# Kernel tuning notes

Hardware: AMD Instinct MI355X
Metric: run time of the kernel (lower is better)

The kernel has to match this reference:

```python
import jax, jax.numpy as jnp
import numpy as np

K_STEPS = 2  # number of staged propagation levels encoded in edge_mask


def _propagate(h, src, dst, mask, num_nodes):
    """KPropagate: K staged scatter-add steps over the edge list.

    Step k sums messages along edges with edge_mask == k; later steps
    propagate the freshly aggregated values (rule-node fan-out).
    """
    out = jnp.zeros_like(h)
    cur = h
    for k in range(K_STEPS):
        msg = jnp.where((mask == k)[:, None], cur[src], jnp.zeros((), h.dtype))  # [E, F]
        out = out + jax.ops.segment_sum(msg, dst, num_segments=num_nodes)
        cur = out
    return out


def setup_inputs() -> dict:
    key = jax.random.key(0)
    ks = jax.random.split(key, 8)
    V, R = 50000, 10000
    N = V + R
    E = 160000
    F_IN, F_OUT = 512, 128
    x = jax.random.normal(ks[0], (N, F_IN), dtype=jnp.float32)
    edge_index = jax.random.randint(ks[1], (2, E), 0, N, dtype=jnp.int64)
    edge_mask = jax.random.randint(ks[2], (E,), 0, K_STEPS, dtype=jnp.int64)
    # lin1: in_features -> in_features; lin2: in_features -> out_features
    s1 = 1.0 / np.sqrt(F_IN)
    W1 = jax.random.uniform(ks[3], (F_IN, F_IN), jnp.float32, -s1, s1)
    b1 = jax.random.uniform(ks[4], (F_IN,), jnp.float32, -s1, s1)
    W2 = jax.random.uniform(ks[5], (F_IN, F_OUT), jnp.float32, -s1, s1)
    b2 = jax.random.uniform(ks[6], (F_OUT,), jnp.float32, -s1, s1)
    return {"x": x, "edge_index": edge_index, "edge_mask": edge_mask,
            "vertex_cnt": V, "rule_cnt": R,
            "W1": W1, "b1": b1, "W2": W2, "b2": b2}


def reference(x, edge_index, edge_mask, vertex_cnt, rule_cnt, W1, b1, W2, b2):
    N = x.shape[0]  # == vertex_cnt + rule_cnt
    src, dst = edge_index[0], edge_index[1]
    h = x @ W1 + b1                                   # lin1
    h = jax.nn.relu(_propagate(h, src, dst, edge_mask, N))  # P1 -> relu
    h = h @ W2 + b2                                   # lin2
    h = _propagate(h, src, dst, edge_mask, N)         # P2
    # NOTE: original code computes log_softmax into `out` but returns x (=h).
    return h
```

## Files before the change

### kernel.cpp

```cpp
#include <hip/hip_runtime.h>

typedef __bf16 bf16x8 __attribute__((ext_vector_type(8)));
typedef float  floatx4 __attribute__((ext_vector_type(4)));
typedef unsigned short ushortx8 __attribute__((ext_vector_type(8)));
typedef unsigned short ushortx4 __attribute__((ext_vector_type(4)));
typedef unsigned short ushortx2 __attribute__((ext_vector_type(2)));

__device__ __forceinline__ float bf2f(unsigned short u) {
    return __uint_as_float(((unsigned)u) << 16);
}
__device__ __forceinline__ unsigned short f2bf(float f) {
    unsigned u = __float_as_uint(f);
    return (unsigned short)((u + 0x7FFFu + ((u >> 16) & 1u)) >> 16);
}

__device__ __forceinline__ void gload_lds16(const unsigned short* g, unsigned short* l) {
    __builtin_amdgcn_global_load_lds(
        (const __attribute__((address_space(1))) void*)g,
        (__attribute__((address_space(3))) void*)l, 16, 0, 0);
}

__global__ void cvt_f32_bf16_kernel(const float* __restrict__ in,
                                    unsigned short* __restrict__ out, int n4) {
    int i = blockIdx.x * blockDim.x + threadIdx.x;
    if (i >= n4) return;
    float4 v = ((const float4*)in)[i];
    ushortx4 o;
    o[0] = f2bf(v.x); o[1] = f2bf(v.y); o[2] = f2bf(v.z); o[3] = f2bf(v.w);
    ((ushortx4*)out)[i] = o;
}

__global__ void transpose_cvt_kernel(const float* __restrict__ in,
                                     unsigned short* __restrict__ out,
                                     int K, int N) {
    int idx = blockIdx.x * blockDim.x + threadIdx.x;
    if (idx >= K * N) return;
    int k = idx / N, n = idx - k * N;
    out[n * K + k] = f2bf(in[idx]);
}

__global__ void init_head_kernel(int* __restrict__ head, int n) {
    int i = blockIdx.x * blockDim.x + threadIdx.x;
    if (i < n) head[i] = -1;
}

__global__ void build_list_kernel(const int* __restrict__ ei, const int* __restrict__ em,
                                  int E, int Nn,
                                  int* __restrict__ head, int* __restrict__ nxt) {
    int e = blockIdx.x * blockDim.x + threadIdx.x;
    if (e >= E) return;
    int d = ei[E + e];
    int m = em[e];
    nxt[e] = atomicExch(&head[m * Nn + d], e);
}

#define BM 128
#define BN 128
#define BK 64

__global__ __launch_bounds__(256) void gemm_bt_bias(
    const unsigned short* __restrict__ A,
    const unsigned short* __restrict__ Bt,
    const float* __restrict__ bias,
    unsigned short* __restrict__ C,
    int M, int N, int K)
{
    __shared__ unsigned short Sh[16384];
    unsigned short (*As)[512] = (unsigned short(*)[512])Sh;
    unsigned short (*Bs)[512] = (unsigned short(*)[512])(Sh + 8192);

    const int tid  = threadIdx.x;
    const int lane = tid & 63;
    const int wave = tid >> 6;

    int bx, by;
    if (gridDim.x == 4) {
        int id = blockIdx.y * 4 + blockIdx.x;
        int full = (gridDim.y & ~7) * 4;
        if (id < full) {
            bx = (id >> 3) & 3;
            by = (id >> 5) * 8 + (id & 7);
        } else {
            int t = id - full;
            by = (gridDim.y & ~7) + (t >> 2);
            bx = t & 3;
        }
    } else {
        bx = blockIdx.x; by = blockIdx.y;
    }
    const int bM = by * BM;
    const int bN = bx * BN;
    const int wm = (wave >> 1) * 64;
    const int wn = (wave & 1) * 64;
    const int q    = lane >> 4;
    const int mrow = lane & 15;

    const unsigned short* pA[4];
    const unsigned short* pB[4];
#pragma unroll
    for (int c = 0; c < 4; c++) {
        int gg = wave + 4 * c;
        int g7 = gg & 7, s = gg >> 3;
        int rA = bM + g7 * 16 + mrow; if (rA >= M) rA = M - 1;
        int rB = bN + g7 * 16 + mrow;
        pA[c] = A  + (size_t)rA * K + s * 32 + q * 8;
        pB[c] = Bt + (size_t)rB * K + s * 32 + q * 8;
    }

    floatx4 acc[4][4];
#pragma unroll
    for (int i = 0; i < 4; i++)
#pragma unroll
        for (int j = 0; j < 4; j++) acc[i][j] = (floatx4)(0.0f);

    for (int kt = 0; kt < K; kt += BK) {
#pragma unroll
        for (int c = 0; c < 4; c++) {
            gload_lds16(pA[c] + kt, &As[wave + 4 * c][0]);
            gload_lds16(pB[c] + kt, &Bs[wave + 4 * c][0]);
        }
        __syncthreads();

#pragma unroll
        for (int s = 0; s < 2; s++) {
            bf16x8 af[4], bfv[4];
#pragma unroll
            for (int mi = 0; mi < 4; mi++)
                af[mi] = *(const bf16x8*)&As[s * 8 + (wave >> 1) * 4 + mi][lane * 8];
#pragma unroll
            for (int ni = 0; ni < 4; ni++)
                bfv[ni] = *(const bf16x8*)&Bs[s * 8 + (wave & 1) * 4 + ni][lane * 8];
#pragma unroll
            for (int mi = 0; mi < 4; mi++)
#pragma unroll
                for (int ni = 0; ni < 4; ni++)
                    acc[mi][ni] = __builtin_amdgcn_mfma_f32_16x16x32_bf16(
                        af[mi], bfv[ni], acc[mi][ni], 0, 0, 0);
        }
        __syncthreads();
    }

    unsigned short* lbuf = Sh + wave * 2048;
    float bv[4];
#pragma unroll
    for (int ni = 0; ni < 4; ni++) bv[ni] = bias[bN + wn + ni * 16 + mrow];

#pragma unroll
    for (int p = 0; p < 2; p++) {
#pragma unroll
        for (int mh = 0; mh < 2; mh++) {
            int mi = 2 * p + mh;
#pragma unroll
            for (int ni = 0; ni < 4; ni++)
#pragma unroll
                for (int r = 0; r < 4; r++)
                    lbuf[(mh * 16 + q * 4 + r) * 64 + ni * 16 + mrow] =
                        f2bf(acc[mi][ni][r] + bv[ni]);
        }
#pragma unroll
        for (int i = 0; i < 4; i++) {
            int prow = i * 8 + (lane >> 3);
            int pcol = (lane & 7) * 8;
            int grow = bM + wm + p * 32 + prow;
            if (grow < M)
                *(ushortx8*)(C + (size_t)grow * N + bN + wn + pcol) =
                    *(const ushortx8*)&lbuf[prow * 64 + pcol];
        }
    }
}

template <int VEC> struct VecT;
template <> struct VecT<8> { typedef ushortx8 type; };
template <> struct VecT<2> { typedef ushortx2 type; };

template <int VEC, bool ADD_SELF, bool RELU, bool OUT_F32>
__global__ __launch_bounds__(256) void prop_step_kernel(
    const unsigned short* __restrict__ cur,
    void* __restrict__ outp,
    const int* __restrict__ head,
    const int* __restrict__ nxt,
    const int* __restrict__ esrc,
    int Nn)
{
    typedef typename VecT<VEC>::type VT;
    const int w = blockIdx.x * 4 + (threadIdx.x >> 6);
    if (w >= Nn) return;
    const int lane = threadIdx.x & 63;
    const int F = VEC * 64;
    const size_t off = (size_t)w * F + lane * VEC;

    float acc[VEC];
    if (ADD_SELF) {
        VT v = *(const VT*)(cur + off);
#pragma unroll
        for (int i = 0; i < VEC; i++) acc[i] = bf2f(v[i]);
    } else {
#pragma unroll
        for (int i = 0; i < VEC; i++) acc[i] = 0.0f;
    }

    for (int e = head[w]; e >= 0; e = nxt[e]) {
        int s = esrc[e];
        VT v = *(const VT*)(cur + (size_t)s * F + lane * VEC);
#pragma unroll
        for (int i = 0; i < VEC; i++) acc[i] += bf2f(v[i]);
    }

#pragma unroll
    for (int i = 0; i < VEC; i++)
        if (RELU && acc[i] < 0.0f) acc[i] = 0.0f;

    if (OUT_F32) {
        float* out = (float*)outp;
        float2 o2;
#pragma unroll
        for (int i = 0; i < VEC; i += 2) {
            o2.x = acc[i]; o2.y = acc[i + 1];
            *(float2*)(out + off + i) = o2;
        }
    } else {
        VT o;
#pragma unroll
        for (int i = 0; i < VEC; i++) o[i] = f2bf(acc[i]);
        *(VT*)((unsigned short*)outp + off) = o;
    }
}

extern "C" void kernel_launch(void* const* d_in, const int* in_sizes, int n_in,
                              void* d_out, int out_size, void* d_ws, size_t ws_size,
                              hipStream_t stream)
{
    const float* x  = (const float*)d_in[0];
    const int*   ei = (const int*)d_in[1];
    const int*   em = (const int*)d_in[2];
    const float* W1 = (const float*)d_in[5];
    const float* b1 = (const float*)d_in[6];
    const float* W2 = (const float*)d_in[7];
    const float* b2 = (const float*)d_in[8];

    const int FIN = 512, FOUT = 128;
    const int Nn = in_sizes[0] / FIN;
    const int E  = in_sizes[2];

    char* ws = (char*)d_ws;
    size_t off = 0;
    auto alloc = [&](size_t bytes) -> char* {
        char* p = ws + off;
        off += (bytes + 255) & ~(size_t)255;
        return p;
    };
    unsigned short* W1t = (unsigned short*)alloc((size_t)FIN * FIN * 2);
    unsigned short* W2t = (unsigned short*)alloc((size_t)FIN * FOUT * 2);
    unsigned short* xb  = (unsigned short*)alloc((size_t)Nn * FIN * 2);
    unsigned short* h1  = (unsigned short*)alloc((size_t)Nn * FIN * 2);
    unsigned short* h2  = (unsigned short*)alloc((size_t)Nn * FOUT * 2);
    unsigned short* A2  = (unsigned short*)alloc((size_t)Nn * FOUT * 2);
    int* head = (int*)alloc((size_t)2 * Nn * 4);
    int* nxt  = (int*)alloc((size_t)E * 4);
    unsigned short* A1 = xb;
    (void)ws_size; (void)n_in; (void)out_size;

    cvt_f32_bf16_kernel<<<((Nn * FIN / 4) + 255) / 256, 256, 0, stream>>>(x, xb, Nn * FIN / 4);
    transpose_cvt_kernel<<<(FIN * FIN + 255) / 256, 256, 0, stream>>>(W1, W1t, FIN, FIN);
    transpose_cvt_kernel<<<(FIN * FOUT + 255) / 256, 256, 0, stream>>>(W2, W2t, FIN, FOUT);

    init_head_kernel<<<(2 * Nn + 255) / 256, 256, 0, stream>>>(head, 2 * Nn);
    build_list_kernel<<<(E + 255) / 256, 256, 0, stream>>>(ei, em, E, Nn, head, nxt);

    {
        dim3 grid(FIN / BN, (Nn + BM - 1) / BM);
        gemm_bt_bias<<<grid, 256, 0, stream>>>(xb, W1t, b1, h1, Nn, FIN, FIN);
    }

    {
        int grid = (Nn + 3) / 4;
        prop_step_kernel<8, false, false, false><<<grid, 256, 0, stream>>>(h1, A1, head,      nxt, ei, Nn);
        prop_step_kernel<8, true,  true,  false><<<grid, 256, 0, stream>>>(A1, h1, head + Nn, nxt, ei, Nn);
    }

    {
        dim3 grid(FOUT / BN, (Nn + BM - 1) / BM);
        gemm_bt_bias<<<grid, 256, 0, stream>>>(h1, W2t, b2, h2, Nn, FOUT, FIN);
    }

    {
        int grid = (Nn + 3) / 4;
        prop_step_kernel<2, false, false, false><<<grid, 256, 0, stream>>>(h2, A2, head,      nxt, ei, Nn);
        prop_step_kernel<2, true,  false, true ><<<grid, 256, 0, stream>>>(A2, d_out, head + Nn, nxt, ei, Nn);
    }
}
```

Before: 398.3 us.

## Double-buffer LDS tiles in bf16 GEMM to overlap loads with MFMA

Splits the GEMM shared-memory tile into two A/B buffer pairs. The loop now issues async global-to-LDS loads for the next K tile while MFMAs run on the current one, with one wait-and-barrier per step instead of two. The goal is to hide global load latency behind compute. In exchange LDS use per block doubles, which can reduce occupancy, and the unrolled schedule assumes an even number of K tiles.

```diff
diff --git a/kernel.cpp b/kernel.cpp
--- a/kernel.cpp
+++ b/kernel.cpp
@@ -65,9 +65,10 @@
     unsigned short* __restrict__ C,
     int M, int N, int K)
 {
-    __shared__ unsigned short Sh[16384];
-    unsigned short (*As)[512] = (unsigned short(*)[512])Sh;
-    unsigned short (*Bs)[512] = (unsigned short(*)[512])(Sh + 8192);
+    __shared__ unsigned short BufA0[8192];
+    __shared__ unsigned short BufB0[8192];
+    __shared__ unsigned short BufA1[8192];
+    __shared__ unsigned short BufB1[8192];
 
     const int tid  = threadIdx.x;
     const int lane = tid & 63;
@@ -113,34 +114,61 @@
 #pragma unroll
         for (int j = 0; j < 4; j++) acc[i][j] = (floatx4)(0.0f);
 
-    for (int kt = 0; kt < K; kt += BK) {
-#pragma unroll
-        for (int c = 0; c < 4; c++) {
-            gload_lds16(pA[c] + kt, &As[wave + 4 * c][0]);
-            gload_lds16(pB[c] + kt, &Bs[wave + 4 * c][0]);
-        }
-        __syncthreads();
-
-#pragma unroll
-        for (int s = 0; s < 2; s++) {
-            bf16x8 af[4], bfv[4];
-#pragma unroll
-            for (int mi = 0; mi < 4; mi++)
-                af[mi] = *(const bf16x8*)&As[s * 8 + (wave >> 1) * 4 + mi][lane * 8];
-#pragma unroll
-            for (int ni = 0; ni < 4; ni++)
-                bfv[ni] = *(const bf16x8*)&Bs[s * 8 + (wave & 1) * 4 + ni][lane * 8];
-#pragma unroll
-            for (int mi = 0; mi < 4; mi++)
-#pragma unroll
-                for (int ni = 0; ni < 4; ni++)
-                    acc[mi][ni] = __builtin_amdgcn_mfma_f32_16x16x32_bf16(
-                        af[mi], bfv[ni], acc[mi][ni], 0, 0, 0);
-        }
-        __syncthreads();
-    }
-
-    unsigned short* lbuf = Sh + wave * 2048;
+#define STAGE(DA, DB, T) do {                                        \
+    const int ko_ = (T) * BK;                                        \
+    _Pragma("unroll")                                                \
+    for (int c_ = 0; c_ < 4; c_++) {                                 \
+        gload_lds16(pA[c_] + ko_, &DA[(wave + 4 * c_) * 512]);       \
+        gload_lds16(pB[c_] + ko_, &DB[(wave + 4 * c_) * 512]);       \
+    }                                                                \
+} while (0)
+
+#define COMPUTE(SA, SB) do {                                                   \
+    _Pragma("unroll")                                                          \
+    for (int s_ = 0; s_ < 2; s_++) {                                           \
+        bf16x8 af[4], bfv[4];                                                  \
+        _Pragma("unroll")                                                      \
+        for (int mi = 0; mi < 4; mi++)                                         \
+            af[mi] = *(const bf16x8*)&SA[(s_ * 8 + (wave >> 1) * 4 + mi) * 512 \
+                                         + lane * 8];                          \
+        _Pragma("unroll")                                                      \
+        for (int ni = 0; ni < 4; ni++)                                         \
+            bfv[ni] = *(const bf16x8*)&SB[(s_ * 8 + (wave & 1) * 4 + ni) * 512 \
+                                          + lane * 8];                         \
+        _Pragma("unroll")                                                      \
+        for (int mi = 0; mi < 4; mi++)                                         \
+            _Pragma("unroll")                                                  \
+            for (int ni = 0; ni < 4; ni++)                                     \
+                acc[mi][ni] = __builtin_amdgcn_mfma_f32_16x16x32_bf16(         \
+                    af[mi], bfv[ni], acc[mi][ni], 0, 0, 0);                    \
+    }                                                                          \
+} while (0)
+
+#define WB asm volatile("s_waitcnt vmcnt(0) lgkmcnt(0)\n\ts_barrier" ::: "memory")
+
+    const int NT = K / BK;
+
+    STAGE(BufA0, BufB0, 0);
+    asm volatile("s_waitcnt vmcnt(0)\n\ts_barrier" ::: "memory");
+
+    for (int t = 1; t + 1 < NT; t += 2) {
+        STAGE(BufA1, BufB1, t);
+        COMPUTE(BufA0, BufB0);
+        WB;
+        STAGE(BufA0, BufB0, t + 1);
+        COMPUTE(BufA1, BufB1);
+        WB;
+    }
+    STAGE(BufA1, BufB1, NT - 1);
+    COMPUTE(BufA0, BufB0);
+    WB;
+    COMPUTE(BufA1, BufB1);
+
+#undef STAGE
+#undef COMPUTE
+#undef WB
+
+    unsigned short* lbuf = BufA0 + wave * 2048;
     float bv[4];
 #pragma unroll
     for (int ni = 0; ni < 4; ni++) bv[ni] = bias[bN + wn + ni * 16 + mrow];
```

Result: no change. 397.4 us (-0.2%).

## Load GEMM fragments directly from global memory instead of staging through LDS

Applied to the files above, without the earlier changes.

Removes the LDS staging (global_load_lds plus two barriers per k-tile) in the bias GEMM. Each wave now loads its A and B MFMA fragments straight from global memory into registers, and shared memory is kept only for the epilogue. This drops the synchronization and LDS traffic, but tiles shared between waves are now fetched redundantly from global/L2, and there is no explicit prefetch to hide load latency.

```diff
diff --git a/kernel.cpp b/kernel.cpp
--- a/kernel.cpp
+++ b/kernel.cpp
@@ -12,12 +12,6 @@
 __device__ __forceinline__ unsigned short f2bf(float f) {
     unsigned u = __float_as_uint(f);
     return (unsigned short)((u + 0x7FFFu + ((u >> 16) & 1u)) >> 16);
-}
-
-__device__ __forceinline__ void gload_lds16(const unsigned short* g, unsigned short* l) {
-    __builtin_amdgcn_global_load_lds(
-        (const __attribute__((address_space(1))) void*)g,
-        (__attribute__((address_space(3))) void*)l, 16, 0, 0);
 }
 
 __global__ void cvt_f32_bf16_kernel(const float* __restrict__ in,
@@ -56,7 +50,6 @@
 
 #define BM 128
 #define BN 128
-#define BK 64
 
 __global__ __launch_bounds__(256) void gemm_bt_bias(
     const unsigned short* __restrict__ A,
@@ -65,9 +58,7 @@
     unsigned short* __restrict__ C,
     int M, int N, int K)
 {
-    __shared__ unsigned short Sh[16384];
-    unsigned short (*As)[512] = (unsigned short(*)[512])Sh;
-    unsigned short (*Bs)[512] = (unsigned short(*)[512])(Sh + 8192);
+    __shared__ unsigned short Ep[8192];
 
     const int tid  = threadIdx.x;
     const int lane = tid & 63;
@@ -95,16 +86,18 @@
     const int q    = lane >> 4;
     const int mrow = lane & 15;
 
-    const unsigned short* pA[4];
-    const unsigned short* pB[4];
-#pragma unroll
-    for (int c = 0; c < 4; c++) {
-        int gg = wave + 4 * c;
-        int g7 = gg & 7, s = gg >> 3;
-        int rA = bM + g7 * 16 + mrow; if (rA >= M) rA = M - 1;
-        int rB = bN + g7 * 16 + mrow;
-        pA[c] = A  + (size_t)rA * K + s * 32 + q * 8;
-        pB[c] = Bt + (size_t)rB * K + s * 32 + q * 8;
+    const unsigned short* ap[4];
+    const unsigned short* bp[4];
+#pragma unroll
+    for (int mi = 0; mi < 4; mi++) {
+        int r = bM + ((wave >> 1) * 4 + mi) * 16 + mrow;
+        if (r >= M) r = M - 1;
+        ap[mi] = A + (size_t)r * K + q * 8;
+    }
+#pragma unroll
+    for (int ni = 0; ni < 4; ni++) {
+        int r = bN + ((wave & 1) * 4 + ni) * 16 + mrow;
+        bp[ni] = Bt + (size_t)r * K + q * 8;
     }
 
     floatx4 acc[4][4];
@@ -113,34 +106,31 @@
 #pragma unroll
         for (int j = 0; j < 4; j++) acc[i][j] = (floatx4)(0.0f);
 
-    for (int kt = 0; kt < K; kt += BK) {
-#pragma unroll
-        for (int c = 0; c < 4; c++) {
-            gload_lds16(pA[c] + kt, &As[wave + 4 * c][0]);
-            gload_lds16(pB[c] + kt, &Bs[wave + 4 * c][0]);
-        }
-        __syncthreads();
-
-#pragma unroll
-        for (int s = 0; s < 2; s++) {
-            bf16x8 af[4], bfv[4];
-#pragma unroll
-            for (int mi = 0; mi < 4; mi++)
-                af[mi] = *(const bf16x8*)&As[s * 8 + (wave >> 1) * 4 + mi][lane * 8];
+    for (int kt = 0; kt < K; kt += 64) {
+        bf16x8 a0[4], a1[4], b0[4], b1[4];
+#pragma unroll
+        for (int mi = 0; mi < 4; mi++) a0[mi] = *(const bf16x8*)(ap[mi] + kt);
+#pragma unroll
+        for (int ni = 0; ni < 4; ni++) b0[ni] = *(const bf16x8*)(bp[ni] + kt);
+#pragma unroll
+        for (int mi = 0; mi < 4; mi++) a1[mi] = *(const bf16x8*)(ap[mi] + kt + 32);
+#pragma unroll
+        for (int ni = 0; ni < 4; ni++) b1[ni] = *(const bf16x8*)(bp[ni] + kt + 32);
+#pragma unroll
+        for (int mi = 0; mi < 4; mi++)
 #pragma unroll
             for (int ni = 0; ni < 4; ni++)
-                bfv[ni] = *(const bf16x8*)&Bs[s * 8 + (wave & 1) * 4 + ni][lane * 8];
-#pragma unroll
-            for (int mi = 0; mi < 4; mi++)
-#pragma unroll
-                for (int ni = 0; ni < 4; ni++)
-                    acc[mi][ni] = __builtin_amdgcn_mfma_f32_16x16x32_bf16(
-                        af[mi], bfv[ni], acc[mi][ni], 0, 0, 0);
-        }
-        __syncthreads();
-    }
-
-    unsigned short* lbuf = Sh + wave * 2048;
+                acc[mi][ni] = __builtin_amdgcn_mfma_f32_16x16x32_bf16(
+                    a0[mi], b0[ni], acc[mi][ni], 0, 0, 0);
+#pragma unroll
+        for (int mi = 0; mi < 4; mi++)
+#pragma unroll
+            for (int ni = 0; ni < 4; ni++)
+                acc[mi][ni] = __builtin_amdgcn_mfma_f32_16x16x32_bf16(
+                    a1[mi], b1[ni], acc[mi][ni], 0, 0, 0);
+    }
+
+    unsigned short* lbuf = Ep + wave * 2048;
     float bv[4];
 #pragma unroll
     for (int ni = 0; ni < 4; ni++) bv[ni] = bias[bN + wn + ni * 16 + mrow];
```

Result: slower. 456.7 us (+14.7%).

## Add 256x256-tile GEMM kernel with 8 waves for the first linear layer

Applied to the files above, without the earlier changes.

Adds a new bf16 MFMA GEMM using 256x256 output tiles, 512 threads and 128x64 per-wave subtiles, with grouped block swizzling for the two-column grid, and uses it for the lin1 GEMM (60000x512x512). Larger tiles raise arithmetic intensity and reduce redundant A/B loads from global memory. The old 128-tile kernel loses its swizzle and keeps only the lin2 GEMM. The trade-off is more registers (128 accumulator floats per thread), lower occupancy, and only about 470 blocks. The single-buffered loop also stalls on a load wait and barrier every k-step.

```diff
diff --git a/kernel.cpp b/kernel.cpp
--- a/kernel.cpp
+++ b/kernel.cpp
@@ -52,6 +52,120 @@
     int d = ei[E + e];
     int m = em[e];
     nxt[e] = atomicExch(&head[m * Nn + d], e);
+}
+
+
+__global__ __launch_bounds__(512) void gemm256_bt_bias(
+    const unsigned short* __restrict__ A,
+    const unsigned short* __restrict__ Bt,
+    const float* __restrict__ bias,
+    unsigned short* __restrict__ C,
+    int M, int N, int K)
+{
+    __shared__ unsigned short As[16384];
+    __shared__ unsigned short Bs[16384];
+
+    const int tid  = threadIdx.x;
+    const int lane = tid & 63;
+    const int wave = tid >> 6;
+
+    int bx, by;
+    if (gridDim.x == 2) {
+        int id = blockIdx.y * 2 + blockIdx.x;
+        int full = (gridDim.y & ~7) * 2;
+        if (id < full) {
+            int grp = id >> 4, w = id & 15;
+            bx = w >> 3;
+            by = grp * 8 + (w & 7);
+        } else {
+            int t = id - full;
+            by = (gridDim.y & ~7) + (t >> 1);
+            bx = t & 1;
+        }
+    } else {
+        bx = blockIdx.x; by = blockIdx.y;
+    }
+    const int bM = by * 256;
+    const int bN = bx * 256;
+    const int wr = wave >> 2;
+    const int wc = wave & 3;
+    const int wm = wr * 128;
+    const int wn = wc * 64;
+    const int q    = lane >> 4;
+    const int mrow = lane & 15;
+
+    const unsigned short* pA[4];
+    const unsigned short* pB[4];
+#pragma unroll
+    for (int c = 0; c < 4; c++) {
+        int gg = wave + 8 * c;
+        int g = gg & 15, s = gg >> 4;
+        int rA = bM + g * 16 + mrow; if (rA >= M) rA = M - 1;
+        int rB = bN + g * 16 + mrow;
+        pA[c] = A  + (size_t)rA * K + s * 32 + q * 8;
+        pB[c] = Bt + (size_t)rB * K + s * 32 + q * 8;
+    }
+
+    floatx4 acc[8][4];
+#pragma unroll
+    for (int i = 0; i < 8; i++)
+#pragma unroll
+        for (int j = 0; j < 4; j++) acc[i][j] = (floatx4)(0.0f);
+
+    for (int kt = 0; kt < K; kt += 64) {
+#pragma unroll
+        for (int c = 0; c < 4; c++) {
+            gload_lds16(pA[c] + kt, &As[(wave + 8 * c) * 512]);
+            gload_lds16(pB[c] + kt, &Bs[(wave + 8 * c) * 512]);
+        }
+        asm volatile("s_waitcnt vmcnt(0)\n\ts_barrier" ::: "memory");
+
+#pragma unroll
+        for (int s = 0; s < 2; s++) {
+            bf16x8 af[8], bfv[4];
+#pragma unroll
+            for (int mi = 0; mi < 8; mi++)
+                af[mi] = *(const bf16x8*)&As[(s * 16 + wr * 8 + mi) * 512 + lane * 8];
+#pragma unroll
+            for (int ni = 0; ni < 4; ni++)
+                bfv[ni] = *(const bf16x8*)&Bs[(s * 16 + wc * 4 + ni) * 512 + lane * 8];
+#pragma unroll
+            for (int mi = 0; mi < 8; mi++)
+#pragma unroll
+                for (int ni = 0; ni < 4; ni++)
+                    acc[mi][ni] = __builtin_amdgcn_mfma_f32_16x16x32_bf16(
+                        af[mi], bfv[ni], acc[mi][ni], 0, 0, 0);
+        }
+        __syncthreads();
+    }
+
+    unsigned short* lbuf = As + wave * 2048;
+    float bv[4];
+#pragma unroll
+    for (int ni = 0; ni < 4; ni++) bv[ni] = bias[bN + wn + ni * 16 + mrow];
+
+#pragma unroll
+    for (int p = 0; p < 4; p++) {
+#pragma unroll
+        for (int mh = 0; mh < 2; mh++) {
+            int mi = 2 * p + mh;
+#pragma unroll
+            for (int ni = 0; ni < 4; ni++)
+#pragma unroll
+                for (int r = 0; r < 4; r++)
+                    lbuf[(mh * 16 + q * 4 + r) * 64 + ni * 16 + mrow] =
+                        f2bf(acc[mi][ni][r] + bv[ni]);
+        }
+#pragma unroll
+        for (int i = 0; i < 4; i++) {
+            int prow = i * 8 + (lane >> 3);
+            int pcol = (lane & 7) * 8;
+            int grow = bM + wm + p * 32 + prow;
+            if (grow < M)
+                *(ushortx8*)(C + (size_t)grow * N + bN + wn + pcol) =
+                    *(const ushortx8*)&lbuf[prow * 64 + pcol];
+        }
+    }
 }
 
 #define BM 128
@@ -73,21 +187,7 @@
     const int lane = tid & 63;
     const int wave = tid >> 6;
 
-    int bx, by;
-    if (gridDim.x == 4) {
-        int id = blockIdx.y * 4 + blockIdx.x;
-        int full = (gridDim.y & ~7) * 4;
-        if (id < full) {
-            bx = (id >> 3) & 3;
-            by = (id >> 5) * 8 + (id & 7);
-        } else {
-            int t = id - full;
-            by = (gridDim.y & ~7) + (t >> 2);
-            bx = t & 3;
-        }
-    } else {
-        bx = blockIdx.x; by = blockIdx.y;
-    }
+    int bx = blockIdx.x, by = blockIdx.y;
     const int bM = by * BM;
     const int bN = bx * BN;
     const int wm = (wave >> 1) * 64;
@@ -268,8 +368,8 @@
     build_list_kernel<<<(E + 255) / 256, 256, 0, stream>>>(ei, em, E, Nn, head, nxt);
 
     {
-        dim3 grid(FIN / BN, (Nn + BM - 1) / BM);
-        gemm_bt_bias<<<grid, 256, 0, stream>>>(xb, W1t, b1, h1, Nn, FIN, FIN);
+        dim3 grid(FIN / 256, (Nn + 255) / 256);
+        gemm256_bt_bias<<<grid, 512, 0, stream>>>(xb, W1t, b1, h1, Nn, FIN, FIN);
     }
 
     {
```

After: 389.7 us. -2.2%, faster.
